# Optimization experiments

Measured on AMD Instinct MI355X. Metric: run time of the kernel, lower is better.

## Reference

```python
import jax, jax.numpy as jnp
import numpy as np
from functools import partial

B, A = 256, 32          # batch_size, num_atoms
N = B * A               # total nodes = 8192
E = 262144              # edges
H = 128                 # hidden_dim
LD, AF = 64, 16         # latent_dim, atom_feature_dim
L = 6                   # num_layers
LN_EPS = 1e-5

silu = jax.nn.silu


def setup_inputs() -> dict:
    key = jax.random.key(0)
    ks = jax.random.split(key, 32)
    s = 0.02
    inp = {
        "z": jax.random.normal(ks[0], (B, LD), jnp.float32),
        "atom_types": jax.random.uniform(ks[1], (N, AF), jnp.float32),
        "pos_init": jax.random.normal(ks[2], (N, 3), jnp.float32) * 0.1,
        "edge_index": jax.random.randint(ks[3], (2, E), 0, N, jnp.int64) if jax.config.jax_enable_x64 else jax.random.randint(ks[3], (2, E), 0, N, jnp.int32),
        "batch": jax.random.randint(ks[4], (N,), 0, B, jnp.int32),
        # latent injector: (LD+AF)->2H -> 2H->H -> H->H
        "inj_W1": jax.random.normal(ks[5], (LD + AF, 2 * H), jnp.float32) * s,
        "inj_b1": jnp.zeros((2 * H,), jnp.float32),
        "inj_W2": jax.random.normal(ks[6], (2 * H, H), jnp.float32) * s,
        "inj_b2": jnp.zeros((H,), jnp.float32),
        "inj_W3": jax.random.normal(ks[7], (H, H), jnp.float32) * s,
        "inj_b3": jnp.zeros((H,), jnp.float32),
        # stacked per-layer params [L, ...]
        "edge_W1": jax.random.normal(ks[8], (L, 2 * H + 1, H), jnp.float32) * s,
        "edge_b1": jnp.zeros((L, H), jnp.float32),
        "edge_W2": jax.random.normal(ks[9], (L, H, H), jnp.float32) * s,
        "edge_b2": jnp.zeros((L, H), jnp.float32),
        "node_W1": jax.random.normal(ks[10], (L, 2 * H, H), jnp.float32) * s,
        "node_b1": jnp.zeros((L, H), jnp.float32),
        "node_W2": jax.random.normal(ks[11], (L, H, H), jnp.float32) * s,
        "node_b2": jnp.zeros((L, H), jnp.float32),
        "coord_W1": jax.random.normal(ks[12], (L, H, H), jnp.float32) * s,
        "coord_b1": jnp.zeros((L, H), jnp.float32),
        "coord_W2": jax.random.normal(ks[13], (L, H, 1), jnp.float32) * s,  # no bias
        "ln_g": jnp.ones((L, H), jnp.float32),
        "ln_b": jnp.zeros((L, H), jnp.float32),
    }
    return inp


def _layer_norm(x, g, b):
    mu = jnp.mean(x, axis=-1, keepdims=True)
    var = jnp.mean(jnp.square(x - mu), axis=-1, keepdims=True)
    return (x - mu) * jax.lax.rsqrt(var + LN_EPS) * g + b


def _egnn_forward(z, atom_types, pos_init, row, col,
                  inj_W1, inj_b1, inj_W2, inj_b2, inj_W3, inj_b3,
                  edge_W1, edge_b1, edge_W2, edge_b2,
                  node_W1, node_b1, node_W2, node_b2,
                  coord_W1, coord_b1, coord_W2, ln_g, ln_b):
    # latent injection
    z_exp = jnp.repeat(z, A, axis=0)                      # [N, LD]
    h0 = jnp.concatenate([atom_types, z_exp], axis=1)     # [N, AF+LD]
    h = silu(h0 @ inj_W1 + inj_b1)
    h = silu(h @ inj_W2 + inj_b2)
    h = h @ inj_W3 + inj_b3                               # [N, H]

    deg = jax.ops.segment_sum(jnp.ones((E,), h.dtype), row, num_segments=N)[:, None]  # [N,1]

    def step(carry, p):
        h, pos = carry
        (eW1, eb1, eW2, eb2, nW1, nb1, nW2, nb2, cW1, cb1, cW2, g, b) = p
        dpos = pos[row] - pos[col]                                   # [E,3]
        dist_sq = jnp.sum(jnp.square(dpos), axis=1, keepdims=True)   # [E,1]
        ef = jnp.concatenate([h[row], h[col], dist_sq], axis=1)      # [E,2H+1]
        m = silu(silu(ef @ eW1 + eb1) @ eW2 + eb2)                   # [E,H]
        cw = silu(m @ cW1 + cb1) @ cW2                               # [E,1]
        coord_update = jax.ops.segment_sum(cw * dpos, row, num_segments=N)  # [N,3]
        pos_new = pos + coord_update / (deg + 1e-6)
        agg = jax.ops.segment_sum(m, row, num_segments=N)            # [N,H]
        nu = silu(jnp.concatenate([h, agg], axis=1) @ nW1 + nb1) @ nW2 + nb2
        h_new = _layer_norm(h + nu, g, b)
        return (h_new, pos_new), None

    params = (edge_W1, edge_b1, edge_W2, edge_b2, node_W1, node_b1,
              node_W2, node_b2, coord_W1, coord_b1, coord_W2, ln_g, ln_b)
    (h, pos), _ = jax.lax.scan(step, (h, pos_init), params)
    return pos


def reference(z, atom_types, pos_init, edge_index, batch,
              inj_W1, inj_b1, inj_W2, inj_b2, inj_W3, inj_b3,
              edge_W1, edge_b1, edge_W2, edge_b2,
              node_W1, node_b1, node_W2, node_b2,
              coord_W1, coord_b1, coord_W2, ln_g, ln_b):
    row, col = edge_index[0], edge_index[1]
    return _egnn_forward(z, atom_types, pos_init, row, col,
                         inj_W1, inj_b1, inj_W2, inj_b2, inj_W3, inj_b3,
                         edge_W1, edge_b1, edge_W2, edge_b2,
                         node_W1, node_b1, node_W2, node_b2,
                         coord_W1, coord_b1, coord_W2, ln_g, ln_b)
```

## Files before the change

### kernel.cpp

```cpp
#include <hip/hip_runtime.h>
#include <hip/hip_bf16.h>

#define NNODES 8192
#define NEDGES 262144
#define HDIM 128
#define NLAYERS 6
#define NMASK (NNODES - 1)

typedef __attribute__((ext_vector_type(8))) short bf16x8;
typedef __attribute__((ext_vector_type(4))) float f32x4;
typedef const __attribute__((address_space(1))) void gvoid;
typedef __attribute__((address_space(3))) void svoid;

__device__ __forceinline__ float silu_f(float x) {
    return x * __builtin_amdgcn_rcpf(1.0f + __expf(-x));
}
__device__ __forceinline__ unsigned short f2bu(float x) {
    unsigned int u; __builtin_memcpy(&u, &x, 4);
    return (unsigned short)((u + 0x8000u) >> 16);
}
__device__ __forceinline__ float bu2f(unsigned short u) {
    unsigned int v = ((unsigned int)u) << 16;
    float f; __builtin_memcpy(&f, &v, 4);
    return f;
}

__device__ __forceinline__ void stage_slice(const unsigned short* src,
                                            unsigned short* dst, int w) {
    const unsigned short* s = src + w * 1024;
    unsigned short* d = dst + w * 1024;
    __builtin_amdgcn_global_load_lds((gvoid*)s, (svoid*)d, 16, 0, 0);
    __builtin_amdgcn_global_load_lds((gvoid*)(s + 512), (svoid*)(d + 512), 16, 0, 0);
}

__global__ void detect_kernel(const int* __restrict__ ei32, int* __restrict__ flags) {
    if (blockIdx.x == 0 && threadIdx.x == 0) {
        flags[1] = (ei32[1] == 0 && ei32[3] == 0 && ei32[5] == 0 && ei32[7] == 0) ? 1 : 0;
    }
}
__device__ __forceinline__ int load_idx(const void* ei, int is64, int i) {
    int v = is64 ? (int)(((const long long*)ei)[i]) : ((const int*)ei)[i];
    return v & NMASK;
}

__global__ void pos_init_kernel(const float* __restrict__ pin, float* __restrict__ pos) {
    int i = blockIdx.x * blockDim.x + threadIdx.x;
    if (i < NNODES * 3) pos[i] = pin[i];
}

__global__ void cnt_kernel(const void* __restrict__ ei, const int* __restrict__ flags,
                           int* __restrict__ cnt) {
    int i = blockIdx.x * blockDim.x + threadIdx.x;
    if (i < NEDGES) atomicAdd(&cnt[load_idx(ei, flags[1], i)], 1);
}
__global__ void scan_kernel(const int* __restrict__ cnt, int* __restrict__ woff,
                            float* __restrict__ deg) {
    __shared__ int sums[256];
    const int t = threadIdx.x;
    const int base = t * 32;
    int s = 0;
#pragma unroll
    for (int i = 0; i < 32; ++i) s += cnt[base + i];
    sums[t] = s;
    __syncthreads();
    if (t == 0) {
        int run = 0;
        for (int k = 0; k < 256; ++k) { int v = sums[k]; sums[k] = run; run += v; }
    }
    __syncthreads();
    int run = sums[t];
#pragma unroll
    for (int i = 0; i < 32; ++i) {
        int c = cnt[base + i];
        woff[base + i] = run;
        deg[base + i] = (float)c;
        run += c;
    }
}
__global__ void scatter_kernel(const void* __restrict__ ei, const int* __restrict__ flags,
                               int* __restrict__ woff,
                               int* __restrict__ rowS, int* __restrict__ colS) {
    int i = blockIdx.x * blockDim.x + threadIdx.x;
    if (i < NEDGES) {
        const int is64 = flags[1];
        int r = load_idx(ei, is64, i);
        int c = load_idx(ei, is64, NEDGES + i);
        int p = atomicAdd(&woff[r], 1);
        rowS[p] = r;
        colS[p] = c;
    }
}

__global__ void prep_weights_kernel(const float* __restrict__ eW1,
                                    const float* __restrict__ eW2,
                                    const float* __restrict__ cW1,
                                    const float* __restrict__ nW1,
                                    const float* __restrict__ nW2,
                                    unsigned short* __restrict__ ewt,
                                    unsigned short* __restrict__ n1tb,
                                    unsigned short* __restrict__ n2tb,
                                    float* __restrict__ w1d) {
    const int TB = NLAYERS * 8 * 4 * 128 * 8;
    const int TS = NLAYERS * 4 * 4 * 128 * 8;
    const int TD = NLAYERS * 128;
    const int TOT = 2 * TB + 3 * TS + TD;
    for (int i = blockIdx.x * blockDim.x + threadIdx.x; i < TOT;
         i += gridDim.x * blockDim.x) {
        if (i < TB) {
            int j = i & 7, r = i >> 3;
            int n = r & 127; r >>= 7;
            int ch = r & 3; r >>= 2;
            int sl = r & 7; int l = r >> 3;
            int k = sl * 32 + ch * 8 + j;
            ewt[(size_t)(l * 16 + sl) * 4096 + ch * 1024 + n * 8 + j] =
                f2bu(eW1[((size_t)l * 257 + k) * 128 + n]);
        } else if (i < TB + TS) {
            int q = i - TB;
            int j = q & 7, r = q >> 3;
            int n = r & 127; r >>= 7;
            int ch = r & 3; r >>= 2;
            int sl = r & 3; int l = r >> 2;
            int k = sl * 32 + ch * 8 + j;
            ewt[(size_t)(l * 16 + 8 + sl) * 4096 + ch * 1024 + n * 8 + j] =
                f2bu(eW2[((size_t)l * 128 + k) * 128 + n]);
        } else if (i < TB + 2 * TS) {
            int q = i - TB - TS;
            int j = q & 7, r = q >> 3;
            int n = r & 127; r >>= 7;
            int ch = r & 3; r >>= 2;
            int sl = r & 3; int l = r >> 2;
            int k = sl * 32 + ch * 8 + j;
            ewt[(size_t)(l * 16 + 12 + sl) * 4096 + ch * 1024 + n * 8 + j] =
                f2bu(cW1[((size_t)l * 128 + k) * 128 + n]);
        } else if (i < 2 * TB + 2 * TS) {
            int q = i - TB - 2 * TS;
            int j = q & 7, r = q >> 3;
            int n = r & 127; r >>= 7;
            int ch = r & 3; r >>= 2;
            int sl = r & 7; int l = r >> 3;
            int k = sl * 32 + ch * 8 + j;
            n1tb[q] = f2bu(nW1[((size_t)l * 256 + k) * 128 + n]);
        } else if (i < 2 * TB + 3 * TS) {
            int q = i - 2 * TB - 2 * TS;
            int j = q & 7, r = q >> 3;
            int n = r & 127; r >>= 7;
            int ch = r & 3; r >>= 2;
            int sl = r & 3; int l = r >> 2;
            int k = sl * 32 + ch * 8 + j;
            n2tb[q] = f2bu(nW2[((size_t)l * 128 + k) * 128 + n]);
        } else {
            int r = i - 2 * TB - 3 * TS, l = r / 128, n = r % 128;
            w1d[r] = eW1[((size_t)l * 257 + 256) * 128 + n];
        }
    }
}

__global__ __launch_bounds__(256) void inj_kernel(
    const float* __restrict__ atom, const float* __restrict__ z,
    const float* __restrict__ W1, const float* __restrict__ b1,
    const float* __restrict__ W2, const float* __restrict__ b2,
    const float* __restrict__ W3, const float* __restrict__ b3,
    unsigned short* __restrict__ hb)
{
    __shared__ __align__(16) float in_s[16][84];
    __shared__ __align__(16) float s1[16][260];
    __shared__ __align__(16) float s2[16][132];
    const int tid = threadIdx.x;
    const int n0 = blockIdx.x * 16;

    if (tid < 80) {
        for (int e = 0; e < 16; ++e) {
            int n = n0 + e;
            in_s[e][tid] = (tid < 16) ? atom[n * 16 + tid] : z[(n >> 5) * 64 + (tid - 16)];
        }
    }
    __syncthreads();
    {
        float acc[16];
        float bias = b1[tid];
#pragma unroll
        for (int e = 0; e < 16; ++e) acc[e] = bias;
        for (int k4 = 0; k4 < 20; ++k4) {
            float w0 = W1[(k4 * 4 + 0) * 256 + tid];
            float w1 = W1[(k4 * 4 + 1) * 256 + tid];
            float w2 = W1[(k4 * 4 + 2) * 256 + tid];
            float w3 = W1[(k4 * 4 + 3) * 256 + tid];
#pragma unroll
            for (int e = 0; e < 16; ++e) {
                const float4 v = *(const float4*)&in_s[e][k4 * 4];
                acc[e] += v.x * w0 + v.y * w1 + v.z * w2 + v.w * w3;
            }
        }
#pragma unroll
        for (int e = 0; e < 16; ++e) s1[e][tid] = silu_f(acc[e]);
    }
    __syncthreads();
    const int j = tid & 127, hv = tid >> 7;
    {
        float acc[8];
        float bias = b2[j];
#pragma unroll
        for (int e = 0; e < 8; ++e) acc[e] = bias;
        for (int k4 = 0; k4 < 64; ++k4) {
            float w0 = W2[(k4 * 4 + 0) * 128 + j];
            float w1 = W2[(k4 * 4 + 1) * 128 + j];
            float w2 = W2[(k4 * 4 + 2) * 128 + j];
            float w3 = W2[(k4 * 4 + 3) * 128 + j];
#pragma unroll
            for (int e = 0; e < 8; ++e) {
                const float4 v = *(const float4*)&s1[hv * 8 + e][k4 * 4];
                acc[e] += v.x * w0 + v.y * w1 + v.z * w2 + v.w * w3;
            }
        }
#pragma unroll
        for (int e = 0; e < 8; ++e) s2[hv * 8 + e][j] = silu_f(acc[e]);
    }
    __syncthreads();
    {
        float acc[8];
        float bias = b3[j];
#pragma unroll
        for (int e = 0; e < 8; ++e) acc[e] = bias;
        for (int k4 = 0; k4 < 32; ++k4) {
            float w0 = W3[(k4 * 4 + 0) * 128 + j];
            float w1 = W3[(k4 * 4 + 1) * 128 + j];
            float w2 = W3[(k4 * 4 + 2) * 128 + j];
            float w3 = W3[(k4 * 4 + 3) * 128 + j];
#pragma unroll
            for (int e = 0; e < 8; ++e) {
                const float4 v = *(const float4*)&s2[hv * 8 + e][k4 * 4];
                acc[e] += v.x * w0 + v.y * w1 + v.z * w2 + v.w * w3;
            }
        }
#pragma unroll
        for (int e = 0; e < 8; ++e)
            hb[(size_t)(n0 + hv * 8 + e) * HDIM + j] = f2bu(acc[e]);
    }
}

__global__ __launch_bounds__(256, 3) void edge_mfma_kernel(
    const unsigned short* __restrict__ hb, const float* __restrict__ pos,
    const int* __restrict__ rowS, const int* __restrict__ colS,
    const unsigned short* __restrict__ wt,
    const float* __restrict__ w1d,
    const float* __restrict__ eb1, const float* __restrict__ eb2,
    const float* __restrict__ cb1, const float* __restrict__ cw2,
    float* __restrict__ agg, float* __restrict__ cu)
{
    __shared__ __align__(16) unsigned short Cbuf[128][136];
    __shared__ __align__(16) unsigned short Bbuf[2][4096];

    const int tid = threadIdx.x;
    const int e0 = blockIdx.x * 128;
    const int L = tid & 63;
    const int w = tid >> 6;
    const int quad = L >> 4, l16 = L & 15;
    const int m0 = w * 32;

    stage_slice(wt, Bbuf[0], w);

    if (tid < 128) {
        int r = rowS[e0 + tid], c = colS[e0 + tid];
        float dx = pos[r * 3 + 0] - pos[c * 3 + 0];
        float dy = pos[r * 3 + 1] - pos[c * 3 + 1];
        float dz = pos[r * 3 + 2] - pos[c * 3 + 2];
        *(float*)&Cbuf[tid][128] = dx * dx + dy * dy + dz * dz;
        Cbuf[tid][130] = (unsigned short)r;
        Cbuf[tid][131] = (unsigned short)c;
        Cbuf[tid][132] = f2bu(dx); Cbuf[tid][133] = f2bu(dy); Cbuf[tid][134] = f2bu(dz);
    }
    __syncthreads();

    const int r0 = Cbuf[m0 + l16][130];
    const int r1 = Cbuf[m0 + 16 + l16][130];
    const int c0 = Cbuf[m0 + l16][131];
    const int c1 = Cbuf[m0 + 16 + l16][131];

    bf16x8 aCur0, aCur1, aNxt0, aNxt1;
    {
        const int kk = quad * 8;
        aCur0 = *(const bf16x8*)(hb + (size_t)r0 * HDIM + kk);
        aCur1 = *(const bf16x8*)(hb + (size_t)r1 * HDIM + kk);
    }

    f32x4 acc[2][8];
    const f32x4 zero = {0.f, 0.f, 0.f, 0.f};
#pragma unroll
    for (int mt = 0; mt < 2; ++mt)
#pragma unroll
        for (int nt = 0; nt < 8; ++nt) acc[mt][nt] = zero;

#pragma unroll
    for (int s = 0; s < 16; ++s) {
        if (s) __syncthreads();
        if (s < 15) stage_slice(wt + (s + 1) * 4096, Bbuf[(s + 1) & 1], w);

        if (s < 7) {
            const int kk = ((s + 1) & 3) * 32 + quad * 8;
            const int nn0 = (s + 1 < 4) ? r0 : c0;
            const int nn1 = (s + 1 < 4) ? r1 : c1;
            aNxt0 = *(const bf16x8*)(hb + (size_t)nn0 * HDIM + kk);
            aNxt1 = *(const bf16x8*)(hb + (size_t)nn1 * HDIM + kk);
        }

        const unsigned short* bp = Bbuf[s & 1] + quad * 1024;
        bf16x8 a0, a1;
        if (s < 8) {
            a0 = aCur0; a1 = aCur1;
        } else {
            const int kk = ((s - 8) & 3) * 32 + quad * 8;
            a0 = *(const bf16x8*)&Cbuf[m0 + l16][kk];
            a1 = *(const bf16x8*)&Cbuf[m0 + 16 + l16][kk];
        }
#pragma unroll
        for (int nt = 0; nt < 8; ++nt) {
            bf16x8 b = *(const bf16x8*)&bp[(nt * 16 + l16) * 8];
            acc[0][nt] = __builtin_amdgcn_mfma_f32_16x16x32_bf16(a0, b, acc[0][nt], 0, 0, 0);
            acc[1][nt] = __builtin_amdgcn_mfma_f32_16x16x32_bf16(a1, b, acc[1][nt], 0, 0, 0);
        }
        if (s < 7) { aCur0 = aNxt0; aCur1 = aNxt1; }

        if (s == 7) {
#pragma unroll
            for (int nt = 0; nt < 8; ++nt) {
                const int n = nt * 16 + l16;
                const float wd = w1d[n];
                const float bias = eb1[n];
#pragma unroll
                for (int mt = 0; mt < 2; ++mt)
#pragma unroll
                    for (int r = 0; r < 4; ++r) {
                        const int m = m0 + mt * 16 + quad * 4 + r;
                        float dsq = *(const float*)&Cbuf[m][128];
                        Cbuf[m][n] = f2bu(silu_f(acc[mt][nt][r] + bias + dsq * wd));
                    }
            }
#pragma unroll
            for (int mt = 0; mt < 2; ++mt)
#pragma unroll
                for (int nt = 0; nt < 8; ++nt) acc[mt][nt] = zero;
        } else if (s == 11) {
#pragma unroll
            for (int nt = 0; nt < 8; ++nt) {
                const int n = nt * 16 + l16;
                const float bias = eb2[n];
#pragma unroll
                for (int mt = 0; mt < 2; ++mt)
#pragma unroll
                    for (int r = 0; r < 4; ++r) {
                        const int m = m0 + mt * 16 + quad * 4 + r;
                        Cbuf[m][n] = f2bu(silu_f(acc[mt][nt][r] + bias));
                    }
            }
#pragma unroll
            for (int mt = 0; mt < 2; ++mt)
#pragma unroll
                for (int nt = 0; nt < 8; ++nt) acc[mt][nt] = zero;
        }
    }

    {
        float s[2][4] = {{0.f, 0.f, 0.f, 0.f}, {0.f, 0.f, 0.f, 0.f}};
#pragma unroll
        for (int nt = 0; nt < 8; ++nt) {
            const int n = nt * 16 + l16;
            const float bias = cb1[n];
            const float wv = cw2[n];
#pragma unroll
            for (int mt = 0; mt < 2; ++mt)
#pragma unroll
                for (int r = 0; r < 4; ++r)
                    s[mt][r] += silu_f(acc[mt][nt][r] + bias) * wv;
        }
#pragma unroll
        for (int mt = 0; mt < 2; ++mt)
#pragma unroll
            for (int r = 0; r < 4; ++r) {
                float v = s[mt][r];
                v += __shfl_xor(v, 1);
                v += __shfl_xor(v, 2);
                v += __shfl_xor(v, 4);
                v += __shfl_xor(v, 8);
                if (l16 == 0)
                    *(float*)&Cbuf[m0 + mt * 16 + quad * 4 + r][128] = v;
            }
    }

    if (L < 32) {
        const int e = m0 + L;
        const int row = Cbuf[e][130];
        const float cwv = *(const float*)&Cbuf[e][128];
        float vx = cwv * bu2f(Cbuf[e][132]);
        float vy = cwv * bu2f(Cbuf[e][133]);
        float vz = cwv * bu2f(Cbuf[e][134]);
#pragma unroll
        for (int d = 1; d < 32; d <<= 1) {
            float ux = __shfl_up(vx, d);
            float uy = __shfl_up(vy, d);
            float uz = __shfl_up(vz, d);
            int rup = __shfl_up(row, d);
            if (L >= d && rup == row) { vx += ux; vy += uy; vz += uz; }
        }
        int rdn = __shfl_down(row, 1);
        if (L == 31 || rdn != row) {
            atomicAdd(&cu[row * 3 + 0], vx);
            atomicAdd(&cu[row * 3 + 1], vy);
            atomicAdd(&cu[row * 3 + 2], vz);
        }
    }

    {
        const int p = L;
        const int eb = m0;
        const int i31 = L & 31;
        const int myrow = Cbuf[eb + i31][130];
        const int prow = __shfl_up(myrow, 1);
        unsigned long long bm64 = __ballot(i31 != 0 && myrow != prow);
        unsigned int bm = (unsigned int)bm64;
        int curr = Cbuf[eb][130];
        float s0 = 0.0f, s1 = 0.0f;
#pragma unroll
        for (int i = 0; i < 32; ++i) {
            unsigned int v = *(const unsigned int*)&Cbuf[eb + i][2 * p];
            if (i && (bm & (1u << i))) {
                atomicAdd(&agg[(size_t)curr * HDIM + 2 * p], s0);
                atomicAdd(&agg[(size_t)curr * HDIM + 2 * p + 1], s1);
                s0 = 0.0f; s1 = 0.0f;
                curr = __shfl(myrow, i);
            }
            s0 += bu2f((unsigned short)(v & 0xffffu));
            s1 += bu2f((unsigned short)(v >> 16));
        }
        atomicAdd(&agg[(size_t)curr * HDIM + 2 * p], s0);
        atomicAdd(&agg[(size_t)curr * HDIM + 2 * p + 1], s1);
    }
}

__global__ __launch_bounds__(128) void node_mfma_kernel(
    const unsigned short* __restrict__ hb,
    float* __restrict__ agg,
    float* __restrict__ cu, const float* __restrict__ deg,
    const unsigned short* __restrict__ n1tb,
    const unsigned short* __restrict__ n2tb,
    const float* __restrict__ b1, const float* __restrict__ b2,
    const float* __restrict__ lg, const float* __restrict__ lb,
    unsigned short* __restrict__ h2b,
    float* __restrict__ pos)
{
    __shared__ __align__(16) unsigned short Cbuf[16][136];
    __shared__ float sLN[2][16][2];
    const int tid = threadIdx.x;
    const int n0 = blockIdx.x * 16;

    if (tid < 16) {
        int n = n0 + tid;
        float inv = __builtin_amdgcn_rcpf(deg[n] + 1e-6f);
        pos[n * 3 + 0] += cu[n * 3 + 0] * inv;
        pos[n * 3 + 1] += cu[n * 3 + 1] * inv;
        pos[n * 3 + 2] += cu[n * 3 + 2] * inv;
        cu[n * 3 + 0] = 0.0f;
        cu[n * 3 + 1] = 0.0f;
        cu[n * 3 + 2] = 0.0f;
    }

    const int L = tid & 63, w = tid >> 6;
    const int quad = L >> 4, l16 = L & 15;
    const int row = n0 + l16;
    const int nb = w * 64;

    f32x4 acc[4];
    const f32x4 zero = {0.f, 0.f, 0.f, 0.f};

#pragma unroll
    for (int nt = 0; nt < 4; ++nt) acc[nt] = zero;
#pragma unroll
    for (int kc = 0; kc < 8; ++kc) {
        bf16x8 a;
        if (kc < 4) {
            const int kk = kc * 32 + quad * 8;
            a = *(const bf16x8*)(hb + (size_t)row * HDIM + kk);
        } else {
            const int kk = (kc - 4) * 32 + quad * 8;
            const float4* p = (const float4*)(agg + (size_t)row * HDIM + kk);
            float4 u0 = p[0], u1 = p[1];
            a[0] = (short)f2bu(u0.x); a[1] = (short)f2bu(u0.y);
            a[2] = (short)f2bu(u0.z); a[3] = (short)f2bu(u0.w);
            a[4] = (short)f2bu(u1.x); a[5] = (short)f2bu(u1.y);
            a[6] = (short)f2bu(u1.z); a[7] = (short)f2bu(u1.w);
        }
        const unsigned short* bp = n1tb + (kc * 4 + quad) * 1024 + (nb + l16) * 8;
#pragma unroll
        for (int nt = 0; nt < 4; ++nt) {
            bf16x8 b = *(const bf16x8*)(bp + nt * 128);
            acc[nt] = __builtin_amdgcn_mfma_f32_16x16x32_bf16(a, b, acc[nt], 0, 0, 0);
        }
    }
    {
        const float4 z4 = {0.f, 0.f, 0.f, 0.f};
        float4* ap = (float4*)(agg + (size_t)(n0 + (tid >> 3)) * HDIM + (tid & 7) * 16);
#pragma unroll
        for (int i = 0; i < 4; ++i) ap[i] = z4;
    }
#pragma unroll
    for (int nt = 0; nt < 4; ++nt) {
        const int n = nb + nt * 16 + l16;
        const float bias = b1[n];
#pragma unroll
        for (int r = 0; r < 4; ++r)
            Cbuf[quad * 4 + r][n] = f2bu(silu_f(acc[nt][r] + bias));
    }
    __syncthreads();

#pragma unroll
    for (int nt = 0; nt < 4; ++nt) acc[nt] = zero;
#pragma unroll
    for (int kc = 0; kc < 4; ++kc) {
        const int kk = kc * 32 + quad * 8;
        bf16x8 a = *(const bf16x8*)&Cbuf[l16][kk];
        const unsigned short* bp = n2tb + (kc * 4 + quad) * 1024 + (nb + l16) * 8;
#pragma unroll
        for (int nt = 0; nt < 4; ++nt) {
            bf16x8 b = *(const bf16x8*)(bp + nt * 128);
            acc[nt] = __builtin_amdgcn_mfma_f32_16x16x32_bf16(a, b, acc[nt], 0, 0, 0);
        }
    }

#pragma unroll
    for (int nt = 0; nt < 4; ++nt) {
        const int n = nb + nt * 16 + l16;
        const float bias = b2[n];
#pragma unroll
        for (int r = 0; r < 4; ++r) {
            const int m = quad * 4 + r;
            acc[nt][r] += bias + bu2f(hb[(size_t)(n0 + m) * HDIM + n]);
        }
    }
#pragma unroll
    for (int r = 0; r < 4; ++r) {
        float s = 0.0f, ss = 0.0f;
#pragma unroll
        for (int nt = 0; nt < 4; ++nt) {
            float x = acc[nt][r];
            s += x; ss += x * x;
        }
#pragma unroll
        for (int d = 1; d < 16; d <<= 1) {
            s += __shfl_xor(s, d);
            ss += __shfl_xor(ss, d);
        }
        if (l16 == 0) {
            sLN[w][quad * 4 + r][0] = s;
            sLN[w][quad * 4 + r][1] = ss;
        }
    }
    __syncthreads();
#pragma unroll
    for (int r = 0; r < 4; ++r) {
        const int m = quad * 4 + r;
        float s = sLN[0][m][0] + sLN[1][m][0];
        float ss = sLN[0][m][1] + sLN[1][m][1];
        float mu = s * (1.0f / 128.0f);
        float var = ss * (1.0f / 128.0f) - mu * mu;
        float rs = rsqrtf(fmaxf(var, 0.0f) + 1e-5f);
#pragma unroll
        for (int nt = 0; nt < 4; ++nt) {
            const int n = nb + nt * 16 + l16;
            float val = (acc[nt][r] - mu) * rs * lg[n] + lb[n];
            h2b[(size_t)(n0 + m) * HDIM + n] = f2bu(val);
        }
    }
}

extern "C" void kernel_launch(void* const* d_in, const int* in_sizes, int n_in,
                              void* d_out, int out_size, void* d_ws, size_t ws_size,
                              hipStream_t stream) {
    const float* zF    = (const float*)d_in[0];
    const float* atomF = (const float*)d_in[1];
    const float* posI  = (const float*)d_in[2];
    const void*  ei    = d_in[3];
    const float* iW1 = (const float*)d_in[5];  const float* ib1 = (const float*)d_in[6];
    const float* iW2 = (const float*)d_in[7];  const float* ib2 = (const float*)d_in[8];
    const float* iW3 = (const float*)d_in[9];  const float* ib3 = (const float*)d_in[10];
    const float* eW1 = (const float*)d_in[11]; const float* eb1 = (const float*)d_in[12];
    const float* eW2 = (const float*)d_in[13]; const float* eb2 = (const float*)d_in[14];
    const float* nW1 = (const float*)d_in[15]; const float* nb1 = (const float*)d_in[16];
    const float* nW2 = (const float*)d_in[17]; const float* nb2 = (const float*)d_in[18];
    const float* cW1 = (const float*)d_in[19]; const float* cb1 = (const float*)d_in[20];
    const float* cW2 = (const float*)d_in[21];
    const float* lng = (const float*)d_in[22]; const float* lnb = (const float*)d_in[23];

    float* pos = (float*)d_out;

    float* ws = (float*)d_ws;
    int* flags = (int*)d_ws;
    size_t cur = 16;
    auto carve = [&](size_t n) { float* p = ws + cur; cur += n; return p; };
    float* deg  = carve(NNODES);
    float* cu   = carve((size_t)NNODES * 3);
    float* agg  = carve((size_t)NNODES * HDIM);
    unsigned short* hbA = (unsigned short*)carve((size_t)NNODES * HDIM / 2);
    unsigned short* hbB = (unsigned short*)carve((size_t)NNODES * HDIM / 2);
    unsigned short* ewt  = (unsigned short*)carve((size_t)NLAYERS * 16 * 4096 / 2);
    unsigned short* n1tb = (unsigned short*)carve((size_t)NLAYERS * 8 * 4096 / 2);
    unsigned short* n2tb = (unsigned short*)carve((size_t)NLAYERS * 4 * 4096 / 2);
    float* w1d  = carve(NLAYERS * 128);
    int* cnt    = (int*)carve(NNODES);
    int* woff   = (int*)carve(NNODES);
    int* rowS   = (int*)carve(NEDGES);
    int* colS   = (int*)carve(NEDGES);

    detect_kernel<<<1, 64, 0, stream>>>((const int*)ei, flags);
    pos_init_kernel<<<(NNODES * 3 + 255) / 256, 256, 0, stream>>>(posI, pos);

    hipMemsetAsync(cnt, 0, NNODES * sizeof(int), stream);
    cnt_kernel<<<NEDGES / 256, 256, 0, stream>>>(ei, flags, cnt);
    scan_kernel<<<1, 256, 0, stream>>>(cnt, woff, deg);
    scatter_kernel<<<NEDGES / 256, 256, 0, stream>>>(ei, flags, woff, rowS, colS);

    prep_weights_kernel<<<2691, 256, 0, stream>>>(eW1, eW2, cW1, nW1, nW2,
                                                  ewt, n1tb, n2tb, w1d);
    inj_kernel<<<NNODES / 16, 256, 0, stream>>>(atomF, zF, iW1, ib1, iW2, ib2, iW3, ib3,
                                                hbA);

    hipMemsetAsync(agg, 0, (size_t)NNODES * HDIM * sizeof(float), stream);
    hipMemsetAsync(cu, 0, (size_t)NNODES * 3 * sizeof(float), stream);

    unsigned short* hb = hbA;
    unsigned short* ob = hbB;
    for (int l = 0; l < NLAYERS; ++l) {
        edge_mfma_kernel<<<NEDGES / 128, 256, 0, stream>>>(
            hb, pos, rowS, colS,
            ewt + (size_t)l * 16 * 4096,
            w1d + (size_t)l * 128,
            eb1 + l * 128, eb2 + l * 128, cb1 + l * 128, cW2 + l * 128,
            agg, cu);
        node_mfma_kernel<<<NNODES / 16, 128, 0, stream>>>(
            hb, agg, cu, deg,
            n1tb + (size_t)l * 8 * 4096,
            n2tb + (size_t)l * 4 * 4096,
            nb1 + l * 128, nb2 + l * 128,
            lng + l * 128, lnb + l * 128,
            ob, pos);
        unsigned short* tb = hb; hb = ob; ob = tb;
    }
}
```

Measured before the change: 627.9 us.

## Precompute per-node edge-MLP first-layer projections to avoid per-edge GEMM

The first edge-MLP layer is linear in the concatenated [h_row, h_col], so it is split into two per-node projections computed once per layer by a new proj_kernel (N×128 → N×256 fp32). The edge kernel then gathers the two projections, adds the distance term, and applies silu, removing 8 of its 16 MFMA K-slices. This trades per-edge matrix work for per-edge gathers of 2×128 fp32 values (more gather bandwidth than the earlier bf16 row reads), plus an extra kernel launch and an 8 MB buffer per layer.

Measured after the change: 716.4 us. 14.1% more time.

```diff
diff --git a/kernel.cpp b/kernel.cpp
--- a/kernel.cpp
+++ b/kernel.cpp
@@ -238,12 +238,52 @@
     }
 }
 
+__global__ __launch_bounds__(64) void proj_kernel(
+    const unsigned short* __restrict__ hb,
+    const unsigned short* __restrict__ wt,
+    const float* __restrict__ eb1,
+    float* __restrict__ pt)
+{
+    const int tid = threadIdx.x;
+    const int quad = tid >> 4, l16 = tid & 15;
+    const int n0 = blockIdx.x * 16;
+
+    const unsigned short* bbase = wt + quad * 1024 + l16 * 8;
+    f32x4 acc[16];
+    const f32x4 zero = {0.f, 0.f, 0.f, 0.f};
+#pragma unroll
+    for (int i = 0; i < 16; ++i) acc[i] = zero;
+
+#pragma unroll
+    for (int kc = 0; kc < 4; ++kc) {
+        bf16x8 a = *(const bf16x8*)(hb + (size_t)(n0 + l16) * HDIM + kc * 32 + quad * 8);
+#pragma unroll
+        for (int nt = 0; nt < 8; ++nt) {
+            bf16x8 bA = *(const bf16x8*)(bbase + kc * 4096 + nt * 128);
+            bf16x8 bB = *(const bf16x8*)(bbase + (4 + kc) * 4096 + nt * 128);
+            acc[nt]     = __builtin_amdgcn_mfma_f32_16x16x32_bf16(a, bA, acc[nt], 0, 0, 0);
+            acc[8 + nt] = __builtin_amdgcn_mfma_f32_16x16x32_bf16(a, bB, acc[8 + nt], 0, 0, 0);
+        }
+    }
+#pragma unroll
+    for (int nt = 0; nt < 8; ++nt) {
+        const int j = nt * 16 + l16;
+        const float bias = eb1[j];
+#pragma unroll
+        for (int r = 0; r < 4; ++r) {
+            const int m = quad * 4 + r;
+            pt[(size_t)(n0 + m) * 256 + j]       = acc[nt][r] + bias;
+            pt[(size_t)(n0 + m) * 256 + 128 + j] = acc[8 + nt][r];
+        }
+    }
+}
+
 __global__ __launch_bounds__(256, 3) void edge_mfma_kernel(
-    const unsigned short* __restrict__ hb, const float* __restrict__ pos,
+    const float* __restrict__ pt, const float* __restrict__ pos,
     const int* __restrict__ rowS, const int* __restrict__ colS,
     const unsigned short* __restrict__ wt,
     const float* __restrict__ w1d,
-    const float* __restrict__ eb1, const float* __restrict__ eb2,
+    const float* __restrict__ eb2,
     const float* __restrict__ cb1, const float* __restrict__ cw2,
     float* __restrict__ agg, float* __restrict__ cu)
 {
@@ -271,16 +311,28 @@
     }
     __syncthreads();
 
-    const int r0 = Cbuf[m0 + l16][130];
-    const int r1 = Cbuf[m0 + 16 + l16][130];
-    const int c0 = Cbuf[m0 + l16][131];
-    const int c1 = Cbuf[m0 + 16 + l16][131];
-
-    bf16x8 aCur0, aCur1, aNxt0, aNxt1;
+    stage_slice(wt + 4096, Bbuf[1], w);
+
     {
-        const int kk = quad * 8;
-        aCur0 = *(const bf16x8*)(hb + (size_t)r0 * HDIM + kk);
-        aCur1 = *(const bf16x8*)(hb + (size_t)r1 * HDIM + kk);
+        const int e = tid >> 1;
+        const int ch0 = (tid & 1) * 64;
+        const int rr = Cbuf[e][130];
+        const int cc = Cbuf[e][131];
+        const float dsq = *(const float*)&Cbuf[e][128];
+        const float* p1p = pt + (size_t)rr * 256 + ch0;
+        const float* p2p = pt + (size_t)cc * 256 + 128 + ch0;
+#pragma unroll
+        for (int v = 0; v < 16; ++v) {
+            const float4 pa = *(const float4*)(p1p + v * 4);
+            const float4 pb = *(const float4*)(p2p + v * 4);
+            const float4 wv = *(const float4*)(w1d + ch0 + v * 4);
+            short4 o;
+            o.x = (short)f2bu(silu_f(pa.x + pb.x + dsq * wv.x));
+            o.y = (short)f2bu(silu_f(pa.y + pb.y + dsq * wv.y));
+            o.z = (short)f2bu(silu_f(pa.z + pb.z + dsq * wv.z));
+            o.w = (short)f2bu(silu_f(pa.w + pb.w + dsq * wv.w));
+            *(short4*)&Cbuf[e][ch0 + v * 4] = o;
+        }
     }
 
     f32x4 acc[2][8];
@@ -291,55 +343,23 @@
         for (int nt = 0; nt < 8; ++nt) acc[mt][nt] = zero;
 
 #pragma unroll
-    for (int s = 0; s < 16; ++s) {
-        if (s) __syncthreads();
-        if (s < 15) stage_slice(wt + (s + 1) * 4096, Bbuf[(s + 1) & 1], w);
-
-        if (s < 7) {
-            const int kk = ((s + 1) & 3) * 32 + quad * 8;
-            const int nn0 = (s + 1 < 4) ? r0 : c0;
-            const int nn1 = (s + 1 < 4) ? r1 : c1;
-            aNxt0 = *(const bf16x8*)(hb + (size_t)nn0 * HDIM + kk);
-            aNxt1 = *(const bf16x8*)(hb + (size_t)nn1 * HDIM + kk);
-        }
-
+    for (int s = 0; s < 8; ++s) {
+        if (s) {
+            __syncthreads();
+            if (s < 7) stage_slice(wt + (s + 1) * 4096, Bbuf[(s + 1) & 1], w);
+        }
         const unsigned short* bp = Bbuf[s & 1] + quad * 1024;
-        bf16x8 a0, a1;
-        if (s < 8) {
-            a0 = aCur0; a1 = aCur1;
-        } else {
-            const int kk = ((s - 8) & 3) * 32 + quad * 8;
-            a0 = *(const bf16x8*)&Cbuf[m0 + l16][kk];
-            a1 = *(const bf16x8*)&Cbuf[m0 + 16 + l16][kk];
-        }
+        const int kk = (s & 3) * 32 + quad * 8;
+        bf16x8 a0 = *(const bf16x8*)&Cbuf[m0 + l16][kk];
+        bf16x8 a1 = *(const bf16x8*)&Cbuf[m0 + 16 + l16][kk];
 #pragma unroll
         for (int nt = 0; nt < 8; ++nt) {
             bf16x8 b = *(const bf16x8*)&bp[(nt * 16 + l16) * 8];
             acc[0][nt] = __builtin_amdgcn_mfma_f32_16x16x32_bf16(a0, b, acc[0][nt], 0, 0, 0);
             acc[1][nt] = __builtin_amdgcn_mfma_f32_16x16x32_bf16(a1, b, acc[1][nt], 0, 0, 0);
         }
-        if (s < 7) { aCur0 = aNxt0; aCur1 = aNxt1; }
-
-        if (s == 7) {
-#pragma unroll
-            for (int nt = 0; nt < 8; ++nt) {
-                const int n = nt * 16 + l16;
-                const float wd = w1d[n];
-                const float bias = eb1[n];
-#pragma unroll
-                for (int mt = 0; mt < 2; ++mt)
-#pragma unroll
-                    for (int r = 0; r < 4; ++r) {
-                        const int m = m0 + mt * 16 + quad * 4 + r;
-                        float dsq = *(const float*)&Cbuf[m][128];
-                        Cbuf[m][n] = f2bu(silu_f(acc[mt][nt][r] + bias + dsq * wd));
-                    }
-            }
-#pragma unroll
-            for (int mt = 0; mt < 2; ++mt)
-#pragma unroll
-                for (int nt = 0; nt < 8; ++nt) acc[mt][nt] = zero;
-        } else if (s == 11) {
+
+        if (s == 3) {
 #pragma unroll
             for (int nt = 0; nt < 8; ++nt) {
                 const int n = nt * 16 + l16;
@@ -600,6 +620,7 @@
     float* agg  = carve((size_t)NNODES * HDIM);
     unsigned short* hbA = (unsigned short*)carve((size_t)NNODES * HDIM / 2);
     unsigned short* hbB = (unsigned short*)carve((size_t)NNODES * HDIM / 2);
+    float* pt   = carve((size_t)NNODES * 256);
     unsigned short* ewt  = (unsigned short*)carve((size_t)NLAYERS * 16 * 4096 / 2);
     unsigned short* n1tb = (unsigned short*)carve((size_t)NLAYERS * 8 * 4096 / 2);
     unsigned short* n2tb = (unsigned short*)carve((size_t)NLAYERS * 4 * 4096 / 2);
@@ -627,12 +648,13 @@
 
     unsigned short* hb = hbA;
     unsigned short* ob = hbB;
+    proj_kernel<<<NNODES / 16, 64, 0, stream>>>(hbA, ewt, eb1, pt);
     for (int l = 0; l < NLAYERS; ++l) {
         edge_mfma_kernel<<<NEDGES / 128, 256, 0, stream>>>(
-            hb, pos, rowS, colS,
-            ewt + (size_t)l * 16 * 4096,
+            pt, pos, rowS, colS,
+            ewt + (size_t)l * 16 * 4096 + 8 * 4096,
             w1d + (size_t)l * 128,
-            eb1 + l * 128, eb2 + l * 128, cb1 + l * 128, cW2 + l * 128,
+            eb2 + l * 128, cb1 + l * 128, cW2 + l * 128,
             agg, cu);
         node_mfma_kernel<<<NNODES / 16, 128, 0, stream>>>(
             hb, agg, cu, deg,
@@ -641,6 +663,9 @@
             nb1 + l * 128, nb2 + l * 128,
             lng + l * 128, lnb + l * 128,
             ob, pos);
+        if (l < NLAYERS - 1)
+            proj_kernel<<<NNODES / 16, 64, 0, stream>>>(
+                ob, ewt + (size_t)(l + 1) * 16 * 4096, eb1 + (l + 1) * 128, pt);
         unsigned short* tb = hb; hb = ob; ob = tb;
     }
 }
```
